# Kernel optimization log

Measured on AMD Instinct MI355X. Metric: run time of the kernel, lower is better.

## Reference

```python
import jax, jax.numpy as jnp
import numpy as np

BLOCK_SPLIT = (4, 4, 4)
GRID = 256
N_BLOCK = 64
BX = GRID // 4  # 64, per-block grid resolution along each axis
N_PTS = 4_194_304


def setup_inputs() -> dict:
    key = jax.random.key(0)
    k1, k2 = jax.random.split(key)
    aabb = jnp.array([[-1.5, -1.5, -1.5], [1.5, 1.5, 1.5]], dtype=jnp.float32)
    # points roughly inside the aabb
    xyz_sampled = jax.random.uniform(k1, (N_PTS, 3), dtype=jnp.float32) * 3.0 - 1.5
    alpha_volume = jax.random.uniform(k2, (GRID, GRID, GRID), dtype=jnp.float32)
    # per-block domains (as kilonerf global_to_local expects): block AABBs
    idx = np.stack(np.meshgrid(np.arange(4), np.arange(4), np.arange(4), indexing='ij'), -1).reshape(-1, 3)
    voxel = np.array([3.0 / 4.0] * 3)
    dmin = (-1.5 + idx * voxel).astype(np.float32)
    dmax = (dmin + voxel).astype(np.float32)
    return {"xyz_sampled": xyz_sampled, "aabb": aabb, "alpha_volume": alpha_volume,
            "domain_min": jnp.asarray(dmin), "domain_max": jnp.asarray(dmax)}


def _sample_alpha(xyz, aabb, alpha_volume, dmin, dmax):
    bs = jnp.asarray(BLOCK_SPLIT, jnp.float32)
    voxel = (aabb[1] - aabb[0]) / bs                      # per-block world size
    idx3 = jnp.floor((xyz - aabb[0]) / voxel).astype(jnp.int32)
    idx3 = jnp.clip(idx3, 0, jnp.array(BLOCK_SPLIT, jnp.int32) - 1)  # edge clamp (matches loop)
    strides = jnp.array([BLOCK_SPLIT[2] * BLOCK_SPLIT[1], BLOCK_SPLIT[2], 1], jnp.int32)
    bid = (idx3 * strides).sum(-1)                        # [N] block id in [0, 64)

    order = jnp.argsort(bid)                              # jax sort is stable; matches bucket-by-block order
    bid_s = bid[order]
    pts = xyz[order]

    # global_to_local (kilonerf): map into per-block [-1,1]^3
    local = 2.0 * (pts - dmin[bid_s]) / (dmax[bid_s] - dmin[bid_s]) - 1.0  # [N,3] (gx,gy,gz)

    # torch .view(64,1,64,64,64) is a raw contiguous reinterpretation -> plain reshape
    vols = alpha_volume.reshape(N_BLOCK, BX, BX, BX)      # [B, D, H, W]
    D = H = W = BX
    # grid_sample convention: grid x -> W axis, y -> H axis, z -> D axis; align_corners=True
    fx = (local[:, 0] + 1.0) * 0.5 * (W - 1)
    fy = (local[:, 1] + 1.0) * 0.5 * (H - 1)
    fz = (local[:, 2] + 1.0) * 0.5 * (D - 1)
    x0 = jnp.floor(fx); y0 = jnp.floor(fy); z0 = jnp.floor(fz)
    wx = fx - x0; wy = fy - y0; wz = fz - z0
    x0i = x0.astype(jnp.int32); y0i = y0.astype(jnp.int32); z0i = z0.astype(jnp.int32)

    def fetch(zi, yi, xi):
        # zeros padding for out-of-range corners (grid_sample padding_mode='zeros')
        inb = (zi >= 0) & (zi < D) & (yi >= 0) & (yi < H) & (xi >= 0) & (xi < W)
        v = vols[bid_s, jnp.clip(zi, 0, D - 1), jnp.clip(yi, 0, H - 1), jnp.clip(xi, 0, W - 1)]
        return jnp.where(inb, v, 0.0)

    out = jnp.zeros_like(fx)
    for dz, wz_ in ((0, 1.0 - wz), (1, wz)):
        for dy, wy_ in ((0, 1.0 - wy), (1, wy)):
            for dx, wx_ in ((0, 1.0 - wx), (1, wx)):
                out = out + wz_ * wy_ * wx_ * fetch(z0i + dz, y0i + dy, x0i + dx)
    return out  # [N] alpha values in block-sorted order


def reference(xyz_sampled, aabb, alpha_volume, domain_min, domain_max):
    return _sample_alpha(xyz_sampled, aabb, alpha_volume, domain_min, domain_max)
```

## Files before the change

### kernel.cpp

```cpp
#include <hip/hip_runtime.h>

#define NB     64
#define NF     4096
#define TILE   16384
#define HBLK   1024
#define DBLK   1024
#define GBLK   256
#define SBLK   256
#define FB_TILE 4096

__device__ __forceinline__ int compute_bid(float px, float py, float pz,
                                           float a0x, float a0y, float a0z,
                                           float vx, float vy, float vz) {
    int ix = (int)floorf((px - a0x) / vx);
    int iy = (int)floorf((py - a0y) / vy);
    int iz = (int)floorf((pz - a0z) / vz);
    ix = min(max(ix, 0), 3);
    iy = min(max(iy, 0), 3);
    iz = min(max(iz, 0), 3);
    return ix * 16 + iy * 4 + iz;
}

__device__ __forceinline__ void quant_point(float px, float py, float pz,
        float a0x, float a0y, float a0z, float vx, float vy, float vz,
        const float* s_dn, const float* s_sc,
        int& b, int& qx, int& qy, int& qz, int& key) {
    b = compute_bid(px, py, pz, a0x, a0y, a0z, vx, vy, vz);
    float fx = (px - s_dn[3 * b])     * s_sc[3 * b];
    float fy = (py - s_dn[3 * b + 1]) * s_sc[3 * b + 1];
    float fz = (pz - s_dn[3 * b + 2]) * s_sc[3 * b + 2];
    qx = min(max(__float2int_rn(fx * 256.0f), 0), 16128);
    qy = min(max(__float2int_rn(fy * 256.0f), 0), 16128);
    qz = min(max(__float2int_rn(fz * 256.0f), 0), 16128);
    key = (b << 6) | ((qz >> 12) << 4) | ((qy >> 12) << 2) | (qx >> 12);
}

__global__ void __launch_bounds__(HBLK) hist_kernel(
        const float* __restrict__ xyz, const float* __restrict__ aabb,
        const float* __restrict__ dmin, const float* __restrict__ dmax,
        int* __restrict__ hist64, int* __restrict__ hist2,
        int* __restrict__ tot4096, int N, int T) {
    __shared__ int   sh[NF];
    __shared__ float s_dn[192], s_sc[192];
    const int tid = threadIdx.x, g = blockIdx.x;
    for (int l = tid; l < NF; l += HBLK) sh[l] = 0;
    if (tid < 192) { s_dn[tid] = dmin[tid]; s_sc[tid] = 63.0f / (dmax[tid] - dmin[tid]); }
    const float a0x = aabb[0], a0y = aabb[1], a0z = aabb[2];
    const float vx = (aabb[3] - a0x) * 0.25f;
    const float vy = (aabb[4] - a0y) * 0.25f;
    const float vz = (aabb[5] - a0z) * 0.25f;
    __syncthreads();
    for (int c = 0; c < TILE / (HBLK * 4); ++c) {
        int p0 = g * TILE + c * (HBLK * 4) + tid * 4;
        int b, qx, qy, qz, k;
        if (p0 + 3 < N) {
            const float4* v4 = (const float4*)(xyz + (size_t)p0 * 3);
            float4 f0 = v4[0], f1 = v4[1], f2 = v4[2];
            quant_point(f0.x, f0.y, f0.z, a0x, a0y, a0z, vx, vy, vz, s_dn, s_sc, b, qx, qy, qz, k);
            atomicAdd(&sh[k], 1);
            quant_point(f0.w, f1.x, f1.y, a0x, a0y, a0z, vx, vy, vz, s_dn, s_sc, b, qx, qy, qz, k);
            atomicAdd(&sh[k], 1);
            quant_point(f1.z, f1.w, f2.x, a0x, a0y, a0z, vx, vy, vz, s_dn, s_sc, b, qx, qy, qz, k);
            atomicAdd(&sh[k], 1);
            quant_point(f2.y, f2.z, f2.w, a0x, a0y, a0z, vx, vy, vz, s_dn, s_sc, b, qx, qy, qz, k);
            atomicAdd(&sh[k], 1);
        } else {
            for (int t = 0; t < 4; ++t) {
                int i = p0 + t;
                if (i < N) {
                    quant_point(xyz[3 * i], xyz[3 * i + 1], xyz[3 * i + 2],
                                a0x, a0y, a0z, vx, vy, vz, s_dn, s_sc, b, qx, qy, qz, k);
                    atomicAdd(&sh[k], 1);
                }
            }
        }
    }
    __syncthreads();
    for (int l = tid; l < NF; l += HBLK) {
        int c = sh[l];
        hist2[(size_t)g * NF + l] = c;
        if (c) atomicAdd(&tot4096[l], c);
    }
    if (tid < NB) {
        int s = 0;
        #pragma unroll
        for (int j = 0; j < 64; ++j) s += sh[tid * 64 + j];
        hist64[tid * T + g] = s;
    }
}

__global__ void scan_rows_kernel(int* __restrict__ hist, int* __restrict__ tot, int G) {
    __shared__ int sh[SBLK];
    const int b = blockIdx.x, t = threadIdx.x;
    const int L = (G + SBLK - 1) / SBLK;
    const int lo = t * L;
    const int n = min(L, max(0, G - lo));
    const int base = b * G + lo;
    int s = 0;
    for (int k = 0; k < n; ++k) s += hist[base + k];
    sh[t] = s;
    __syncthreads();
    for (int off = 1; off < SBLK; off <<= 1) {
        int v = (t >= off) ? sh[t - off] : 0;
        __syncthreads();
        sh[t] += v;
        __syncthreads();
    }
    int excl = (t == 0) ? 0 : sh[t - 1];
    for (int k = 0; k < n; ++k) {
        int v = hist[base + k];
        hist[base + k] = excl;
        excl += v;
    }
    if (t == SBLK - 1) tot[b] = sh[SBLK - 1];
}

__global__ void fscan_kernel(const int* __restrict__ tot4096,
                             int* __restrict__ foff, int* __restrict__ fcnt) {
    __shared__ int sh[SBLK];
    const int t = threadIdx.x;
    const int L = NF / SBLK;
    int loc[16];
    int s = 0;
    #pragma unroll
    for (int j = 0; j < L; ++j) { loc[j] = tot4096[t * L + j]; s += loc[j]; }
    sh[t] = s;
    __syncthreads();
    for (int o = 1; o < SBLK; o <<= 1) {
        int v = (t >= o) ? sh[t - o] : 0;
        __syncthreads();
        sh[t] += v;
        __syncthreads();
    }
    int run = (t == 0) ? 0 : sh[t - 1];
    #pragma unroll
    for (int j = 0; j < L; ++j) {
        foff[t * L + j] = run;
        fcnt[t * L + j] = run;
        run += loc[j];
    }
    if (t == SBLK - 1) foff[NF] = run;
}

__global__ void __launch_bounds__(DBLK) scatterD_kernel(
        const float* __restrict__ xyz, const float* __restrict__ aabb,
        const float* __restrict__ dmin, const float* __restrict__ dmax,
        const int* __restrict__ hist64, const int* __restrict__ tot64,
        const int* __restrict__ hist2, int* __restrict__ fcnt,
        unsigned long long* __restrict__ payloadF, int N, int T) {
    __shared__ int   s_fb[NF];
    __shared__ int   s_wh[16][NB];
    __shared__ int   s_cnt0[NB];
    __shared__ int   s_off[NB];
    __shared__ float s_dn[192], s_sc[192];
    const int tid = threadIdx.x, g = blockIdx.x;
    const int lane = tid & 63, wv = tid >> 6;
    for (int l = tid; l < NF; l += DBLK) {
        int c = hist2[(size_t)g * NF + l];
        s_fb[l] = c ? atomicAdd(&fcnt[l], c) : 0;
    }
    if (tid < NB) s_off[tid] = tot64[tid];
    if (tid < 192) { s_dn[tid] = dmin[tid]; s_sc[tid] = 63.0f / (dmax[tid] - dmin[tid]); }
    ((int*)s_wh)[tid] = 0;
    const float a0x = aabb[0], a0y = aabb[1], a0z = aabb[2];
    const float vx = (aabb[3] - a0x) * 0.25f;
    const float vy = (aabb[4] - a0y) * 0.25f;
    const float vz = (aabb[5] - a0z) * 0.25f;
    __syncthreads();
    for (int o = 1; o < NB; o <<= 1) {
        int v = (tid < NB && tid >= o) ? s_off[tid - o] : 0;
        __syncthreads();
        if (tid < NB) s_off[tid] += v;
        __syncthreads();
    }
    if (tid < NB) s_cnt0[tid] = hist64[tid * T + g] + (tid ? s_off[tid - 1] : 0);

    const unsigned long long lt = (1ull << lane) - 1ull;
    const int base_i = g * TILE + wv * 1024;
    unsigned long long cache[16];
    #pragma unroll
    for (int r = 0; r < 16; ++r) {
        int i = base_i + r * 64 + lane;
        bool valid = (i < N);
        int b = 0, qx = 0, qy = 0, qz = 0, key;
        if (valid) {
            quant_point(xyz[3 * i], xyz[3 * i + 1], xyz[3 * i + 2],
                        a0x, a0y, a0z, vx, vy, vz, s_dn, s_sc, b, qx, qy, qz, key);
        }
        unsigned long long m = __ballot(valid);
        #pragma unroll
        for (int q = 0; q < 6; ++q) {
            unsigned long long bal = __ballot((b >> q) & 1);
            m &= ((b >> q) & 1) ? bal : ~bal;
        }
        int rank = __popcll(m & lt);
        int run = valid ? s_wh[wv][b] : 0;
        if (valid && rank == 0) s_wh[wv][b] = run + __popcll(m);
        int localpos = run + rank;
        cache[r] = (unsigned long long)(unsigned)qx
                 | ((unsigned long long)(unsigned)qy << 14)
                 | ((unsigned long long)(unsigned)qz << 28)
                 | ((unsigned long long)(unsigned)b  << 42)
                 | ((unsigned long long)(unsigned)localpos << 48);
    }
    __syncthreads();
    for (int o = 1; o < 16; o <<= 1) {
        int v = (wv >= o) ? s_wh[wv - o][lane] : 0;
        __syncthreads();
        s_wh[wv][lane] += v;
        __syncthreads();
    }
    #pragma unroll
    for (int r = 0; r < 16; ++r) {
        int i = base_i + r * 64 + lane;
        if (i < N) {
            unsigned long long cc = cache[r];
            int qx = (int)(cc & 16383), qy = (int)((cc >> 14) & 16383);
            int qz = (int)((cc >> 28) & 16383);
            int b = (int)((cc >> 42) & 63);
            int localpos = (int)((cc >> 48) & 1023);
            int pos = s_cnt0[b] + (wv ? s_wh[wv - 1][b] : 0) + localpos;
            int key = (b << 6) | ((qz >> 12) << 4) | ((qy >> 12) << 2) | (qx >> 12);
            int fpos = atomicAdd(&s_fb[key], 1);
            payloadF[fpos] = (unsigned long long)(unsigned)qx
                           | ((unsigned long long)(unsigned)qy << 14)
                           | ((unsigned long long)(unsigned)qz << 28)
                           | ((unsigned long long)(unsigned)pos << 42);
        }
    }
}

__global__ void __launch_bounds__(GBLK) gather_kernel(
        const float* __restrict__ vol,
        const unsigned long long* __restrict__ payloadF,
        const int* __restrict__ foff, float* __restrict__ out) {
    __shared__ float sv[17 * 17 * 17];
    const int tid = threadIdx.x;
    const int nb = gridDim.x, d = blockIdx.x;
    const int k = (nb % 8 == 0) ? (d % 8) * (nb / 8) + (d / 8) : d;
    const int b = k >> 6;
    const int bz = ((k >> 4) & 3) * 16, by = ((k >> 2) & 3) * 16, bx = (k & 3) * 16;
    const float* vb = vol + ((size_t)b << 18);
    for (int l = tid; l < 17 * 17 * 17; l += GBLK) {
        int z = l / 289, r = l - z * 289, y = r / 17, x = r - y * 17;
        int gz = bz + z, gy = by + y, gx = bx + x;
        sv[l] = (gz < 64 && gy < 64 && gx < 64)
                    ? vb[(gz << 12) + (gy << 6) + gx] : 0.0f;
    }
    __syncthreads();
    const int lo = foff[k];
    const int n = foff[k + 1] - lo;
    for (int j = tid; j < n; j += GBLK) {
        unsigned long long p = payloadF[lo + j];
        int qx = (int)(p & 16383), qy = (int)((p >> 14) & 16383);
        int qz = (int)((p >> 28) & 16383);
        int pos = (int)(p >> 42);
        float wx = (qx & 255) * (1.0f / 256.0f);
        float wy = (qy & 255) * (1.0f / 256.0f);
        float wz = (qz & 255) * (1.0f / 256.0f);
        int lx = (qx >> 8) - bx, ly = (qy >> 8) - by, lz = (qz >> 8) - bz;
        int base = lz * 289 + ly * 17 + lx;
        float v000 = sv[base],       v001 = sv[base + 1];
        float v010 = sv[base + 17],  v011 = sv[base + 18];
        float v100 = sv[base + 289], v101 = sv[base + 290];
        float v110 = sv[base + 306], v111 = sv[base + 307];
        float c00 = v000 + wx * (v001 - v000);
        float c01 = v010 + wx * (v011 - v010);
        float c10 = v100 + wx * (v101 - v100);
        float c11 = v110 + wx * (v111 - v110);
        float c0 = c00 + wy * (c01 - c00);
        float c1 = c10 + wy * (c11 - c10);
        out[pos] = c0 + wz * (c1 - c0);
    }
}

__global__ void fb_hist_kernel(const float* __restrict__ xyz,
                               const float* __restrict__ aabb,
                               int* __restrict__ hist, int N, int G) {
    __shared__ int s_h[NB];
    const int tid = threadIdx.x, g = blockIdx.x;
    if (tid < NB) s_h[tid] = 0;
    __syncthreads();
    const float a0x = aabb[0], a0y = aabb[1], a0z = aabb[2];
    const float vx = (aabb[3] - a0x) * 0.25f;
    const float vy = (aabb[4] - a0y) * 0.25f;
    const float vz = (aabb[5] - a0z) * 0.25f;
    for (int c = 0; c < FB_TILE / 256; ++c) {
        int i = g * FB_TILE + c * 256 + tid;
        if (i < N)
            atomicAdd(&s_h[compute_bid(xyz[3 * i], xyz[3 * i + 1], xyz[3 * i + 2],
                                       a0x, a0y, a0z, vx, vy, vz)], 1);
    }
    __syncthreads();
    if (tid < NB) hist[tid * G + g] = s_h[tid];
}

__global__ void fb_scatter_kernel(const float* __restrict__ xyz,
                                  const float* __restrict__ aabb,
                                  const float* __restrict__ dmin,
                                  const float* __restrict__ dmax,
                                  const float* __restrict__ vol,
                                  const int* __restrict__ hist,
                                  const int* __restrict__ tot64,
                                  float* __restrict__ out, int N, int G) {
    __shared__ int   s_cnt[NB], s_off[NB];
    __shared__ int   s_whist[4][NB];
    __shared__ float s_dn[192], s_sc[192];
    const int tid = threadIdx.x, g = blockIdx.x;
    if (tid < NB) s_off[tid] = tot64[tid];
    if (tid < 192) { s_dn[tid] = dmin[tid]; s_sc[tid] = 63.0f / (dmax[tid] - dmin[tid]); }
    __syncthreads();
    for (int o = 1; o < NB; o <<= 1) {
        int v = (tid < NB && tid >= o) ? s_off[tid - o] : 0;
        __syncthreads();
        if (tid < NB) s_off[tid] += v;
        __syncthreads();
    }
    if (tid < NB) s_cnt[tid] = hist[tid * G + g] + (tid ? s_off[tid - 1] : 0);
    const float a0x = aabb[0], a0y = aabb[1], a0z = aabb[2];
    const float vx = (aabb[3] - a0x) * 0.25f;
    const float vy = (aabb[4] - a0y) * 0.25f;
    const float vz = (aabb[5] - a0z) * 0.25f;
    __syncthreads();
    const int lane = tid & 63, wv = tid >> 6;
    const unsigned long long lt = (1ull << lane) - 1ull;
    for (int c = 0; c < FB_TILE / 256; ++c) {
        int i = g * FB_TILE + c * 256 + tid;
        bool valid = (i < N);
        int b = 0;
        float alpha = 0.0f;
        if (valid) {
            float px = xyz[3 * i], py = xyz[3 * i + 1], pz = xyz[3 * i + 2];
            b = compute_bid(px, py, pz, a0x, a0y, a0z, vx, vy, vz);
            float fx = (px - s_dn[3 * b])     * s_sc[3 * b];
            float fy = (py - s_dn[3 * b + 1]) * s_sc[3 * b + 1];
            float fz = (pz - s_dn[3 * b + 2]) * s_sc[3 * b + 2];
            float x0f = floorf(fx), y0f = floorf(fy), z0f = floorf(fz);
            float wx = fx - x0f, wy = fy - y0f, wz = fz - z0f;
            int x0 = (int)x0f, y0 = (int)y0f, z0 = (int)z0f;
            const float* vb = vol + ((size_t)b << 18);
            auto F = [&](int zi, int yi, int xi) -> float {
                if ((unsigned)zi >= 64u || (unsigned)yi >= 64u || (unsigned)xi >= 64u)
                    return 0.0f;
                return vb[(zi << 12) + (yi << 6) + xi];
            };
            float s = 0.0f;
            s += (1.0f - wz) * (1.0f - wy) * (1.0f - wx) * F(z0,     y0,     x0);
            s += (1.0f - wz) * (1.0f - wy) * wx          * F(z0,     y0,     x0 + 1);
            s += (1.0f - wz) * wy          * (1.0f - wx) * F(z0,     y0 + 1, x0);
            s += (1.0f - wz) * wy          * wx          * F(z0,     y0 + 1, x0 + 1);
            s += wz          * (1.0f - wy) * (1.0f - wx) * F(z0 + 1, y0,     x0);
            s += wz          * (1.0f - wy) * wx          * F(z0 + 1, y0,     x0 + 1);
            s += wz          * wy          * (1.0f - wx) * F(z0 + 1, y0 + 1, x0);
            s += wz          * wy          * wx          * F(z0 + 1, y0 + 1, x0 + 1);
            alpha = s;
        }
        ((int*)s_whist)[tid] = 0;
        __syncthreads();
        unsigned long long m = __ballot(valid);
        #pragma unroll
        for (int q = 0; q < 6; ++q) {
            unsigned long long bal = __ballot((b >> q) & 1);
            m &= ((b >> q) & 1) ? bal : ~bal;
        }
        int rank = __popcll(m & lt);
        if (valid && rank == 0) s_whist[wv][b] = __popcll(m);
        __syncthreads();
        if (valid) {
            int pos = s_cnt[b] + rank;
            for (int w2 = 0; w2 < wv; ++w2) pos += s_whist[w2][b];
            out[pos] = alpha;
        }
        __syncthreads();
        if (tid < NB)
            s_cnt[tid] += s_whist[0][tid] + s_whist[1][tid] +
                          s_whist[2][tid] + s_whist[3][tid];
        __syncthreads();
    }
}

extern "C" void kernel_launch(void* const* d_in, const int* in_sizes, int n_in,
                              void* d_out, int out_size, void* d_ws, size_t ws_size,
                              hipStream_t stream) {
    const float* xyz  = (const float*)d_in[0];
    const float* aabb = (const float*)d_in[1];
    const float* vol  = (const float*)d_in[2];
    const float* dmin = (const float*)d_in[3];
    const float* dmax = (const float*)d_in[4];
    float* out = (float*)d_out;
    const int N = in_sizes[0] / 3;
    const int T = (N + TILE - 1) / TILE;

    auto align = [](size_t x) { return (x + 255) & ~(size_t)255; };
    char* ws = (char*)d_ws;
    size_t o = 0;
    unsigned long long* payloadF = (unsigned long long*)(ws + o); o += align((size_t)N * 8);
    int* hist64  = (int*)(ws + o); o += align((size_t)NB * T * 4);
    int* tot64   = (int*)(ws + o); o += 256;
    int* hist2   = (int*)(ws + o); o += align((size_t)T * NF * 4);
    int* tot4096 = (int*)(ws + o); o += align((size_t)NF * 4);
    int* foff    = (int*)(ws + o); o += align((size_t)(NF + 1) * 4);
    int* fcnt    = (int*)(ws + o); o += align((size_t)NF * 4);
    const bool fine = (N <= (1 << 22)) && (ws_size >= o);

    if (fine) {
        hipMemsetAsync(tot4096, 0, NF * 4, stream);
        hist_kernel<<<T, HBLK, 0, stream>>>(xyz, aabb, dmin, dmax,
                                            hist64, hist2, tot4096, N, T);
        scan_rows_kernel<<<NB, SBLK, 0, stream>>>(hist64, tot64, T);
        fscan_kernel<<<1, SBLK, 0, stream>>>(tot4096, foff, fcnt);
        scatterD_kernel<<<T, DBLK, 0, stream>>>(xyz, aabb, dmin, dmax, hist64,
                                                tot64, hist2, fcnt, payloadF, N, T);
        gather_kernel<<<NF, GBLK, 0, stream>>>(vol, payloadF, foff, out);
    } else {
        const int Gf = (N + FB_TILE - 1) / FB_TILE;
        int* h = (int*)ws;
        int* t = (int*)(ws + align((size_t)NB * Gf * 4));
        fb_hist_kernel<<<Gf, 256, 0, stream>>>(xyz, aabb, h, N, Gf);
        scan_rows_kernel<<<NB, SBLK, 0, stream>>>(h, t, Gf);
        fb_scatter_kernel<<<Gf, 256, 0, stream>>>(xyz, aabb, dmin, dmax, vol,
                                                  h, t, out, N, Gf);
    }
}
```

Measured before the change: 280.1 us.

## Split scatter into coarse block-sorted pass and separate fine-bucket scatter

Drops the per-tile 4096-bin histogram array (hist2) that the histogram pass wrote and the scatter pass read back. The scatter now runs in two stages: the first writes a block-sorted coarse payload, and a new kernel re-histograms each tile locally in shared memory, reserves global fine-bucket offsets, and writes the fine-sorted payload. The two scan kernels are also merged into one launch. In exchange, an extra N-sized 64-bit payload is written to global memory and read twice. The order of points within a fine bucket can also change, since it now comes from atomic arrival order.

```diff
diff --git a/kernel.cpp b/kernel.cpp
--- a/kernel.cpp
+++ b/kernel.cpp
@@ -5,6 +5,7 @@
 #define TILE   16384
 #define HBLK   1024
 #define DBLK   1024
+#define FBLK   512
 #define GBLK   256
 #define SBLK   256
 #define FB_TILE 4096
@@ -38,8 +39,7 @@
 __global__ void __launch_bounds__(HBLK) hist_kernel(
         const float* __restrict__ xyz, const float* __restrict__ aabb,
         const float* __restrict__ dmin, const float* __restrict__ dmax,
-        int* __restrict__ hist64, int* __restrict__ hist2,
-        int* __restrict__ tot4096, int N, int T) {
+        int* __restrict__ hist64, int* __restrict__ tot4096, int N, int T) {
     __shared__ int   sh[NF];
     __shared__ float s_dn[192], s_sc[192];
     const int tid = threadIdx.x, g = blockIdx.x;
@@ -78,7 +78,6 @@
     __syncthreads();
     for (int l = tid; l < NF; l += HBLK) {
         int c = sh[l];
-        hist2[(size_t)g * NF + l] = c;
         if (c) atomicAdd(&tot4096[l], c);
     }
     if (tid < NB) {
@@ -89,76 +88,70 @@
     }
 }
 
-__global__ void scan_rows_kernel(int* __restrict__ hist, int* __restrict__ tot, int G) {
-    __shared__ int sh[SBLK];
-    const int b = blockIdx.x, t = threadIdx.x;
-    const int L = (G + SBLK - 1) / SBLK;
-    const int lo = t * L;
-    const int n = min(L, max(0, G - lo));
-    const int base = b * G + lo;
-    int s = 0;
-    for (int k = 0; k < n; ++k) s += hist[base + k];
-    sh[t] = s;
-    __syncthreads();
-    for (int off = 1; off < SBLK; off <<= 1) {
-        int v = (t >= off) ? sh[t - off] : 0;
-        __syncthreads();
-        sh[t] += v;
-        __syncthreads();
-    }
-    int excl = (t == 0) ? 0 : sh[t - 1];
-    for (int k = 0; k < n; ++k) {
-        int v = hist[base + k];
-        hist[base + k] = excl;
-        excl += v;
-    }
-    if (t == SBLK - 1) tot[b] = sh[SBLK - 1];
-}
-
-__global__ void fscan_kernel(const int* __restrict__ tot4096,
-                             int* __restrict__ foff, int* __restrict__ fcnt) {
+__global__ void scans_kernel(int* __restrict__ hist64, int* __restrict__ tot64,
+                             const int* __restrict__ tot4096,
+                             int* __restrict__ foff, int* __restrict__ fcnt, int G) {
     __shared__ int sh[SBLK];
     const int t = threadIdx.x;
-    const int L = NF / SBLK;
-    int loc[16];
-    int s = 0;
-    #pragma unroll
-    for (int j = 0; j < L; ++j) { loc[j] = tot4096[t * L + j]; s += loc[j]; }
-    sh[t] = s;
-    __syncthreads();
-    for (int o = 1; o < SBLK; o <<= 1) {
-        int v = (t >= o) ? sh[t - o] : 0;
-        __syncthreads();
-        sh[t] += v;
-        __syncthreads();
-    }
-    int run = (t == 0) ? 0 : sh[t - 1];
-    #pragma unroll
-    for (int j = 0; j < L; ++j) {
-        foff[t * L + j] = run;
-        fcnt[t * L + j] = run;
-        run += loc[j];
-    }
-    if (t == SBLK - 1) foff[NF] = run;
-}
-
-__global__ void __launch_bounds__(DBLK) scatterD_kernel(
+    if (blockIdx.x < NB) {
+        const int b = blockIdx.x;
+        const int L = (G + SBLK - 1) / SBLK;
+        const int lo = t * L;
+        const int n = min(L, max(0, G - lo));
+        const int base = b * G + lo;
+        int s = 0;
+        for (int k = 0; k < n; ++k) s += hist64[base + k];
+        sh[t] = s;
+        __syncthreads();
+        for (int off = 1; off < SBLK; off <<= 1) {
+            int v = (t >= off) ? sh[t - off] : 0;
+            __syncthreads();
+            sh[t] += v;
+            __syncthreads();
+        }
+        int excl = (t == 0) ? 0 : sh[t - 1];
+        for (int k = 0; k < n; ++k) {
+            int v = hist64[base + k];
+            hist64[base + k] = excl;
+            excl += v;
+        }
+        if (t == SBLK - 1) tot64[b] = sh[SBLK - 1];
+    } else {
+        const int L = NF / SBLK;
+        int loc[16];
+        int s = 0;
+        #pragma unroll
+        for (int j = 0; j < L; ++j) { loc[j] = tot4096[t * L + j]; s += loc[j]; }
+        sh[t] = s;
+        __syncthreads();
+        for (int o = 1; o < SBLK; o <<= 1) {
+            int v = (t >= o) ? sh[t - o] : 0;
+            __syncthreads();
+            sh[t] += v;
+            __syncthreads();
+        }
+        int run = (t == 0) ? 0 : sh[t - 1];
+        #pragma unroll
+        for (int j = 0; j < L; ++j) {
+            foff[t * L + j] = run;
+            fcnt[t * L + j] = run;
+            run += loc[j];
+        }
+        if (t == SBLK - 1) foff[NF] = run;
+    }
+}
+
+__global__ void __launch_bounds__(DBLK) scatterC_kernel(
         const float* __restrict__ xyz, const float* __restrict__ aabb,
         const float* __restrict__ dmin, const float* __restrict__ dmax,
         const int* __restrict__ hist64, const int* __restrict__ tot64,
-        const int* __restrict__ hist2, int* __restrict__ fcnt,
-        unsigned long long* __restrict__ payloadF, int N, int T) {
-    __shared__ int   s_fb[NF];
+        unsigned long long* __restrict__ payloadC, int N, int T) {
     __shared__ int   s_wh[16][NB];
     __shared__ int   s_cnt0[NB];
     __shared__ int   s_off[NB];
     __shared__ float s_dn[192], s_sc[192];
     const int tid = threadIdx.x, g = blockIdx.x;
     const int lane = tid & 63, wv = tid >> 6;
-    for (int l = tid; l < NF; l += DBLK) {
-        int c = hist2[(size_t)g * NF + l];
-        s_fb[l] = c ? atomicAdd(&fcnt[l], c) : 0;
-    }
     if (tid < NB) s_off[tid] = tot64[tid];
     if (tid < 192) { s_dn[tid] = dmin[tid]; s_sc[tid] = 63.0f / (dmax[tid] - dmin[tid]); }
     ((int*)s_wh)[tid] = 0;
@@ -215,18 +208,45 @@
         int i = base_i + r * 64 + lane;
         if (i < N) {
             unsigned long long cc = cache[r];
-            int qx = (int)(cc & 16383), qy = (int)((cc >> 14) & 16383);
-            int qz = (int)((cc >> 28) & 16383);
             int b = (int)((cc >> 42) & 63);
             int localpos = (int)((cc >> 48) & 1023);
             int pos = s_cnt0[b] + (wv ? s_wh[wv - 1][b] : 0) + localpos;
-            int key = (b << 6) | ((qz >> 12) << 4) | ((qy >> 12) << 2) | (qx >> 12);
-            int fpos = atomicAdd(&s_fb[key], 1);
-            payloadF[fpos] = (unsigned long long)(unsigned)qx
-                           | ((unsigned long long)(unsigned)qy << 14)
-                           | ((unsigned long long)(unsigned)qz << 28)
-                           | ((unsigned long long)(unsigned)pos << 42);
-        }
+            payloadC[pos] = cc & ((1ull << 48) - 1);
+        }
+    }
+}
+
+__global__ void __launch_bounds__(FBLK) scatterF_kernel(
+        const unsigned long long* __restrict__ payloadC,
+        int* __restrict__ fcnt,
+        unsigned long long* __restrict__ payloadF, int N) {
+    __shared__ int s_fb[NF];
+    const int tid = threadIdx.x, t2 = blockIdx.x;
+    for (int l = tid; l < NF; l += FBLK) s_fb[l] = 0;
+    __syncthreads();
+    const int lo = t2 * TILE;
+    const int n = min(TILE, N - lo);
+    for (int j = tid; j < n; j += FBLK) {
+        unsigned long long p = payloadC[lo + j];
+        int qx = (int)(p & 16383), qy = (int)((p >> 14) & 16383);
+        int qz = (int)((p >> 28) & 16383), b = (int)((p >> 42) & 63);
+        int key = (b << 6) | ((qz >> 12) << 4) | ((qy >> 12) << 2) | (qx >> 12);
+        atomicAdd(&s_fb[key], 1);
+    }
+    __syncthreads();
+    for (int l = tid; l < NF; l += FBLK) {
+        int c = s_fb[l];
+        s_fb[l] = c ? atomicAdd(&fcnt[l], c) : 0;
+    }
+    __syncthreads();
+    for (int j = tid; j < n; j += FBLK) {
+        unsigned long long p = payloadC[lo + j];
+        int qx = (int)(p & 16383), qy = (int)((p >> 14) & 16383);
+        int qz = (int)((p >> 28) & 16383), b = (int)((p >> 42) & 63);
+        int key = (b << 6) | ((qz >> 12) << 4) | ((qy >> 12) << 2) | (qx >> 12);
+        int fpos = atomicAdd(&s_fb[key], 1);
+        payloadF[fpos] = (p & ((1ull << 42) - 1))
+                       | ((unsigned long long)(unsigned)(lo + j) << 42);
     }
 }
 
@@ -293,6 +313,32 @@
     }
     __syncthreads();
     if (tid < NB) hist[tid * G + g] = s_h[tid];
+}
+
+__global__ void fb_scan_kernel(int* __restrict__ hist, int* __restrict__ tot, int G) {
+    __shared__ int sh[SBLK];
+    const int b = blockIdx.x, t = threadIdx.x;
+    const int L = (G + SBLK - 1) / SBLK;
+    const int lo = t * L;
+    const int n = min(L, max(0, G - lo));
+    const int base = b * G + lo;
+    int s = 0;
+    for (int k = 0; k < n; ++k) s += hist[base + k];
+    sh[t] = s;
+    __syncthreads();
+    for (int off = 1; off < SBLK; off <<= 1) {
+        int v = (t >= off) ? sh[t - off] : 0;
+        __syncthreads();
+        sh[t] += v;
+        __syncthreads();
+    }
+    int excl = (t == 0) ? 0 : sh[t - 1];
+    for (int k = 0; k < n; ++k) {
+        int v = hist[base + k];
+        hist[base + k] = excl;
+        excl += v;
+    }
+    if (t == SBLK - 1) tot[b] = sh[SBLK - 1];
 }
 
 __global__ void fb_scatter_kernel(const float* __restrict__ xyz,
@@ -394,10 +440,10 @@
     auto align = [](size_t x) { return (x + 255) & ~(size_t)255; };
     char* ws = (char*)d_ws;
     size_t o = 0;
+    unsigned long long* payloadC = (unsigned long long*)(ws + o); o += align((size_t)N * 8);
     unsigned long long* payloadF = (unsigned long long*)(ws + o); o += align((size_t)N * 8);
     int* hist64  = (int*)(ws + o); o += align((size_t)NB * T * 4);
     int* tot64   = (int*)(ws + o); o += 256;
-    int* hist2   = (int*)(ws + o); o += align((size_t)T * NF * 4);
     int* tot4096 = (int*)(ws + o); o += align((size_t)NF * 4);
     int* foff    = (int*)(ws + o); o += align((size_t)(NF + 1) * 4);
     int* fcnt    = (int*)(ws + o); o += align((size_t)NF * 4);
@@ -406,18 +452,19 @@
     if (fine) {
         hipMemsetAsync(tot4096, 0, NF * 4, stream);
         hist_kernel<<<T, HBLK, 0, stream>>>(xyz, aabb, dmin, dmax,
-                                            hist64, hist2, tot4096, N, T);
-        scan_rows_kernel<<<NB, SBLK, 0, stream>>>(hist64, tot64, T);
-        fscan_kernel<<<1, SBLK, 0, stream>>>(tot4096, foff, fcnt);
-        scatterD_kernel<<<T, DBLK, 0, stream>>>(xyz, aabb, dmin, dmax, hist64,
-                                                tot64, hist2, fcnt, payloadF, N, T);
+                                            hist64, tot4096, N, T);
+        scans_kernel<<<NB + 1, SBLK, 0, stream>>>(hist64, tot64, tot4096,
+                                                  foff, fcnt, T);
+        scatterC_kernel<<<T, DBLK, 0, stream>>>(xyz, aabb, dmin, dmax,
+                                                hist64, tot64, payloadC, N, T);
+        scatterF_kernel<<<T, FBLK, 0, stream>>>(payloadC, fcnt, payloadF, N);
         gather_kernel<<<NF, GBLK, 0, stream>>>(vol, payloadF, foff, out);
     } else {
         const int Gf = (N + FB_TILE - 1) / FB_TILE;
         int* h = (int*)ws;
         int* t = (int*)(ws + align((size_t)NB * Gf * 4));
         fb_hist_kernel<<<Gf, 256, 0, stream>>>(xyz, aabb, h, N, Gf);
-        scan_rows_kernel<<<NB, SBLK, 0, stream>>>(h, t, Gf);
+        fb_scan_kernel<<<NB, SBLK, 0, stream>>>(h, t, Gf);
         fb_scatter_kernel<<<Gf, 256, 0, stream>>>(xyz, aabb, dmin, dmax, vol,
                                                   h, t, out, N, Gf);
     }
```

New measurement: 279.3 us. No clear change (-0.3%).
